# Performance work log

Measured on AMD Instinct MI355X. Metric: run time of the kernel, lower is better.

## Reference

```python
import jax, jax.numpy as jnp
import numpy as np

# Config (matches init_kwargs)
HQ, HKV, HD, WIN = 16, 4, 128, 512  # query heads, kv heads, head_dim, sliding window


def setup_inputs() -> dict:
    key = jax.random.key(0)
    k0, k1, k2, k3, k4 = jax.random.split(key, 5)
    B, S, D = 1, 8192, 2048
    std = 0.02
    hidden_states = jax.random.normal(k0, (B, S, D), jnp.float32)
    Wq = jax.random.normal(k1, (D, HQ * HD), jnp.float32) * std
    Wk = jax.random.normal(k2, (D, HKV * HD), jnp.float32) * std
    Wv = jax.random.normal(k3, (D, HKV * HD), jnp.float32) * std
    Wo = jax.random.normal(k4, (HQ * HD, D), jnp.float32) * std
    return {"hidden_states": hidden_states, "Wq": Wq, "Wk": Wk, "Wv": Wv, "Wo": Wo}


def _sliding_window_attention(q, k, v, win):
    # block i attend to keys of blocks i-1 and i -> scores [B,H,nb,W,2W].
    B, H, S, hd = q.shape
    W = win
    nb = S // W
    qb = q.reshape(B, H, nb, W, hd)
    kpad = jnp.pad(k, ((0, 0), (0, 0), (W, 0), (0, 0)))
    vpad = jnp.pad(v, ((0, 0), (0, 0), (W, 0), (0, 0)))
    kb = jnp.concatenate([kpad[:, :, :S].reshape(B, H, nb, W, hd),
                          k.reshape(B, H, nb, W, hd)], axis=3)  # [B,H,nb,2W,hd]
    vb = jnp.concatenate([vpad[:, :, :S].reshape(B, H, nb, W, hd),
                          v.reshape(B, H, nb, W, hd)], axis=3)
    # Faithful double-scaling of the source: /sqrt(hd) inside the chunk matmul
    # and again before softmax -> effective /hd.
    scores = jnp.einsum('bhnqd,bhnkd->bhnqk', qb, kb) / jnp.asarray(hd, qb.dtype)
    qi = jnp.arange(W)[:, None]
    ki = jnp.arange(2 * W)[None, :]
    # key local index k maps to global offset (k - W) relative to block start;
    # attend iff 0 <= q_glob - k_glob <= W-1  <=>  q+1 <= k <= q+W
    band = (ki >= qi + 1) & (ki <= qi + W)          # [W, 2W]
    blk = jnp.arange(nb)[:, None, None]
    valid = band[None] & ((blk > 0) | (ki[None] >= W))  # block 0 has no prev keys
    neg = jnp.finfo(scores.dtype).min
    scores = jnp.where(valid[None, None], scores, neg)
    probs = jax.nn.softmax(scores, axis=-1)
    out = jnp.einsum('bhnqk,bhnkd->bhnqd', probs, vb)
    return out.reshape(B, H, S, hd)


def reference(hidden_states, Wq, Wk, Wv, Wo):
    B, S, D = hidden_states.shape
    q = (hidden_states @ Wq).reshape(B, S, HQ, HD).transpose(0, 2, 1, 3)
    k = (hidden_states @ Wk).reshape(B, S, HKV, HD).transpose(0, 2, 1, 3)
    v = (hidden_states @ Wv).reshape(B, S, HKV, HD).transpose(0, 2, 1, 3)
    rep = HQ // HKV
    k = jnp.repeat(k, rep, axis=1)
    v = jnp.repeat(v, rep, axis=1)
    attn = _sliding_window_attention(q, k, v, WIN)      # [B,HQ,S,HD]
    attn = attn.transpose(0, 2, 1, 3).reshape(B, S, HQ * HD)
    return attn @ Wo
```

## Files before the change

### kernel.cpp

```cpp
#include <hip/hip_runtime.h>


typedef __bf16 bf16x8 __attribute__((ext_vector_type(8)));
typedef float f32x4 __attribute__((ext_vector_type(4)));
typedef float f32x16 __attribute__((ext_vector_type(16)));
typedef int v8i __attribute__((ext_vector_type(8)));
typedef unsigned int u32x4 __attribute__((ext_vector_type(4)));

__device__ __forceinline__ unsigned short f2bf(float f) {
  unsigned int u = __float_as_uint(f);
  u += 0x7fffu + ((u >> 16) & 1u);
  return (unsigned short)(u >> 16);
}

__device__ __forceinline__ f32x4 mfma16(bf16x8 a, bf16x8 b, f32x4 c) {
  return __builtin_amdgcn_mfma_f32_16x16x32_bf16(a, b, c, 0, 0, 0);
}

__device__ __forceinline__ f32x16 mfma32(bf16x8 a, bf16x8 b, f32x16 c) {
  return __builtin_amdgcn_mfma_f32_32x32x16_bf16(a, b, c, 0, 0, 0);
}

__device__ __forceinline__ unsigned int cvtpk_bf16(float lo, float hi) {
  unsigned int r;
  asm volatile("v_cvt_pk_bf16_f32 %0, %1, %2" : "=v"(r) : "v"(lo), "v"(hi));
  return r;
}

__device__ __forceinline__ void async16(void* lds, const void* g) {
  __builtin_amdgcn_global_load_lds(
      (__attribute__((address_space(1))) unsigned int*)g,
      (__attribute__((address_space(3))) unsigned int*)lds, 16, 0, 0);
}


__global__ __launch_bounds__(256) void convert_h_kernel(
    const float* __restrict__ src, unsigned short* __restrict__ dbf,
    unsigned char* __restrict__ d8, int n) {
  int i = (blockIdx.x * 256 + threadIdx.x) * 4;
  if (i < n) {
    float4 f = *(const float4*)(src + i);
    ushort4 o;
    o.x = f2bf(f.x); o.y = f2bf(f.y); o.z = f2bf(f.z); o.w = f2bf(f.w);
    *(ushort4*)(dbf + i) = o;
    int p = __builtin_amdgcn_cvt_pk_fp8_f32(f.x, f.y, 0, 0);
    p = __builtin_amdgcn_cvt_pk_fp8_f32(f.z, f.w, p, 1);
    *(unsigned int*)(d8 + i) = p;
  }
}

__global__ __launch_bounds__(256) void transpose_convert_kernel(
    const float* __restrict__ src, unsigned short* __restrict__ dst,
    int K, int N) {
  __shared__ unsigned short T[64 * 72];
  int kb = blockIdx.y * 64, nb = blockIdx.x * 64;
  int t = threadIdx.x;
  for (int u = t; u < 1024; u += 256) {
    int r = u >> 4, s = u & 15;
    float4 f = *(const float4*)(src + (size_t)(kb + r) * N + nb + s * 4);
    ushort4 o;
    o.x = f2bf(f.x); o.y = f2bf(f.y); o.z = f2bf(f.z); o.w = f2bf(f.w);
    *(ushort4*)&T[r * 72 + s * 4] = o;
  }
  __syncthreads();
  for (int u = t; u < 1024; u += 256) {
    int orow = u >> 4, s = u & 15;
    ushort4 o;
    o.x = T[(s * 4 + 0) * 72 + orow];
    o.y = T[(s * 4 + 1) * 72 + orow];
    o.z = T[(s * 4 + 2) * 72 + orow];
    o.w = T[(s * 4 + 3) * 72 + orow];
    *(ushort4*)(dst + (size_t)(nb + orow) * K + kb + s * 4) = o;
  }
}

__global__ __launch_bounds__(256) void transpose_convert_fp8_kernel(
    const float* __restrict__ src, unsigned char* __restrict__ dst,
    int K, int N) {
  __shared__ unsigned short T[64 * 72];
  int kb = blockIdx.y * 64, nb = blockIdx.x * 64;
  int t = threadIdx.x;
  for (int u = t; u < 1024; u += 256) {
    int r = u >> 4, s = u & 15;
    float4 f = *(const float4*)(src + (size_t)(kb + r) * N + nb + s * 4);
    ushort4 o;
    o.x = f2bf(f.x); o.y = f2bf(f.y); o.z = f2bf(f.z); o.w = f2bf(f.w);
    *(ushort4*)&T[r * 72 + s * 4] = o;
  }
  __syncthreads();
  for (int u = t; u < 1024; u += 256) {
    int orow = u >> 4, s = u & 15;
    float f0 = __uint_as_float((unsigned int)T[(s * 4 + 0) * 72 + orow] << 16);
    float f1 = __uint_as_float((unsigned int)T[(s * 4 + 1) * 72 + orow] << 16);
    float f2 = __uint_as_float((unsigned int)T[(s * 4 + 2) * 72 + orow] << 16);
    float f3 = __uint_as_float((unsigned int)T[(s * 4 + 3) * 72 + orow] << 16);
    int p = __builtin_amdgcn_cvt_pk_fp8_f32(f0, f1, 0, 0);
    p = __builtin_amdgcn_cvt_pk_fp8_f32(f2, f3, p, 1);
    *(unsigned int*)&dst[(size_t)(nb + orow) * K + kb + s * 4] = p;
  }
}

__global__ __launch_bounds__(256) void vtrans_kernel(
    const unsigned short* __restrict__ QKV, unsigned short* __restrict__ VTg) {
  int flat = blockIdx.x * 256 + threadIdx.x;
  int c = flat & 511;
  int s0 = (flat >> 9) * 8;
  unsigned short tmp[8];
  #pragma unroll
  for (int j = 0; j < 8; ++j)
    tmp[j] = QKV[(size_t)(s0 + j) * 3072 + 2560 + c];
  *(uint4*)&VTg[(size_t)c * 8192 + s0] = *(uint4*)tmp;
}


template <bool F32OUT>
__global__ __launch_bounds__(256) void gemm_bt_kernel(
    const unsigned short* __restrict__ A, const unsigned short* __restrict__ BT,
    void* __restrict__ Cp, int M, int ldc, int K) {
  __shared__ unsigned short As[128 * 32];
  __shared__ unsigned short Bs[128 * 32];
  int mb = blockIdx.y * 128, nb = blockIdx.x * 128;
  int tid = threadIdx.x;
  int lane = tid & 63, wv = tid >> 6;
  int wrow = wv >> 1, wcol = wv & 1;
  int lr = lane >> 2, ls = lane & 3;
  int fr = lane & 15, fg = lane >> 4;
  f32x4 acc[4][4] = {};
  for (int k0 = 0; k0 < K; k0 += 32) {
    __syncthreads();
    #pragma unroll
    for (int r = 0; r < 2; ++r) {
      int s = wv * 2 + r;
      async16(&As[s * 512], &A[(size_t)(mb + s * 16 + lr) * K + k0 + ls * 8]);
      async16(&Bs[s * 512], &BT[(size_t)(nb + s * 16 + lr) * K + k0 + ls * 8]);
    }
    __syncthreads();
    bf16x8 a[4], b[4];
    #pragma unroll
    for (int rt = 0; rt < 4; ++rt)
      a[rt] = *(const bf16x8*)&As[(wrow * 64 + rt * 16 + fr) * 32 + fg * 8];
    #pragma unroll
    for (int ct = 0; ct < 4; ++ct)
      b[ct] = *(const bf16x8*)&Bs[(wcol * 64 + ct * 16 + fr) * 32 + fg * 8];
    #pragma unroll
    for (int rt = 0; rt < 4; ++rt)
      #pragma unroll
      for (int ct = 0; ct < 4; ++ct)
        acc[rt][ct] = mfma16(a[rt], b[ct], acc[rt][ct]);
  }
  #pragma unroll
  for (int rt = 0; rt < 4; ++rt)
    #pragma unroll
    for (int ct = 0; ct < 4; ++ct)
      #pragma unroll
      for (int i = 0; i < 4; ++i) {
        int row = mb + wrow * 64 + rt * 16 + fg * 4 + i;
        int col = nb + wcol * 64 + ct * 16 + fr;
        if constexpr (F32OUT)
          ((float*)Cp)[(size_t)row * ldc + col] = acc[rt][ct][i];
        else
          ((unsigned short*)Cp)[(size_t)row * ldc + col] = f2bf(acc[rt][ct][i]);
      }
}


__global__ __launch_bounds__(512, 2) void gemm8p_oproj_kernel(
    const unsigned short* __restrict__ A, const unsigned short* __restrict__ BT,
    float* __restrict__ C, int ldc, int K) {
  __shared__ unsigned char lds[131072];
  const int mb = blockIdx.y * 256, nb = blockIdx.x * 256;
  const int tid = threadIdx.x;
  const int lane = tid & 63, wv = tid >> 6;
  const int wm = wv >> 2, wn = wv & 3;
  const int fr = lane & 15, fg = lane >> 4;
  const int xr = (fr & 4) ? 32 : 0;
  const int a_base = (wm * 128 + fr) * 128 + ((fg * 16) ^ xr);
  const int b_base = (wn * 64 + fr) * 128 + ((fg * 16) ^ xr);
  const int lsw = (lane * 16) ^ (lane & 32);
  const int lrow = lsw >> 7, lcol = (lsw & 127) >> 1;
  const int NT = K >> 6;

  f32x4 acc[8][4] = {};
  bf16x8 aF[4][2], bF[2][2];

#define FENCE_ asm volatile("" ::: "memory")
#define BAR_ { FENCE_; __builtin_amdgcn_s_barrier(); FENCE_; }
#define LGKM0_ asm volatile("s_waitcnt lgkmcnt(0)" ::: "memory")
#define STAGE_A_(BUFI, T, HALF)                                              \
  { _Pragma("unroll")                                                        \
    for (int l = 0; l < 2; ++l) {                                            \
      int cc = wv * 2 + l;                                                   \
      int rb = (cc >> 3) * 128 + (HALF) * 64 + (cc & 7) * 8;                 \
      async16(lds + (BUFI) * 65536 + rb * 128,                               \
              A + (size_t)(mb + rb + lrow) * K + (T) * 64 + lcol);           \
    } }
#define STAGE_B_(BUFI, T, HALF)                                              \
  { _Pragma("unroll")                                                        \
    for (int l = 0; l < 2; ++l) {                                            \
      int cc = wv * 2 + l;                                                   \
      int rb = (cc >> 2) * 64 + (HALF) * 32 + (cc & 3) * 8;                  \
      async16(lds + (BUFI) * 65536 + 32768 + rb * 128,                       \
              BT + (size_t)(nb + rb + lrow) * K + (T) * 64 + lcol);          \
    } }
#define LOAD_A_(HALF)                                                        \
  { _Pragma("unroll")                                                        \
    for (int q = 0; q < 4; ++q)                                              \
      _Pragma("unroll")                                                      \
      for (int kk = 0; kk < 2; ++kk)                                         \
        aF[q][kk] =                                                          \
            *(const bf16x8*)&Ab_[a_base + ((HALF)*4 + q) * 2048 + kk * 64]; }
#define LOAD_B_(HALF)                                                        \
  { _Pragma("unroll")                                                        \
    for (int c2 = 0; c2 < 2; ++c2)                                           \
      _Pragma("unroll")                                                      \
      for (int kk = 0; kk < 2; ++kk)                                         \
        bF[c2][kk] =                                                         \
            *(const bf16x8*)&Bb_[b_base + ((HALF)*2 + c2) * 2048 + kk * 64]; }
#define MFMA_(RT0, CT0)                                                      \
  { __builtin_amdgcn_s_setprio(1);                                           \
    _Pragma("unroll")                                                        \
    for (int q = 0; q < 4; ++q)                                              \
      _Pragma("unroll")                                                      \
      for (int c2 = 0; c2 < 2; ++c2) {                                       \
        acc[(RT0) + q][(CT0) + c2] =                                         \
            mfma16(aF[q][0], bF[c2][0], acc[(RT0) + q][(CT0) + c2]);         \
        acc[(RT0) + q][(CT0) + c2] =                                         \
            mfma16(aF[q][1], bF[c2][1], acc[(RT0) + q][(CT0) + c2]);         \
      }                                                                      \
    __builtin_amdgcn_s_setprio(0); }

  STAGE_A_(0, 0, 0); STAGE_A_(0, 0, 1); STAGE_B_(0, 0, 0); STAGE_B_(0, 0, 1);
  STAGE_B_(1, 1, 0); STAGE_A_(1, 1, 1);
  asm volatile("s_waitcnt vmcnt(4)" ::: "memory");
  BAR_;

  for (int t = 0; t < NT; ++t) {
    const int cur = t & 1, nxt = cur ^ 1;
    const unsigned char* Ab_ = lds + cur * 65536;
    const unsigned char* Bb_ = Ab_ + 32768;
    LOAD_A_(0); LOAD_B_(0);
    if (t + 1 < NT) STAGE_A_(nxt, t + 1, 0);
    BAR_; LGKM0_;
    MFMA_(0, 0);
    BAR_;
    LOAD_A_(1);
    if (t + 1 < NT) STAGE_B_(nxt, t + 1, 1);
    BAR_; LGKM0_;
    MFMA_(4, 0);
    BAR_;
    LOAD_B_(1);
    if (t + 2 < NT) STAGE_B_(cur, t + 2, 0);
    BAR_; LGKM0_;
    MFMA_(4, 2);
    BAR_;
    LOAD_A_(0);
    if (t + 2 < NT) STAGE_A_(cur, t + 2, 1);
    BAR_; LGKM0_;
    MFMA_(0, 2);
    asm volatile("s_waitcnt vmcnt(4)" ::: "memory");
    BAR_;
  }

  #pragma unroll
  for (int rt = 0; rt < 8; ++rt)
    #pragma unroll
    for (int ct = 0; ct < 4; ++ct)
      #pragma unroll
      for (int i = 0; i < 4; ++i) {
        int row = mb + wm * 128 + rt * 16 + fg * 4 + i;
        int col = nb + wn * 64 + ct * 16 + fr;
        C[(size_t)row * ldc + col] = acc[rt][ct][i];
      }
#undef FENCE_
#undef BAR_
#undef LGKM0_
#undef STAGE_A_
#undef STAGE_B_
#undef LOAD_A_
#undef LOAD_B_
#undef MFMA_
}


__global__ __launch_bounds__(256) void gemm_qk_fp8_kernel(
    const unsigned char* __restrict__ A8, const unsigned char* __restrict__ B8,
    unsigned short* __restrict__ C, int M, int ldc, int K) {
  __shared__ unsigned char As[128 * 144];
  __shared__ unsigned char Bs[128 * 144];
  int mb = blockIdx.y * 128, nb = blockIdx.x * 128;
  int tid = threadIdx.x;
  int lane = tid & 63, wv = tid >> 6;
  int wrow = wv >> 1, wcol = wv & 1;
  int fr = lane & 15, fg = lane >> 4;
  int srow = tid >> 1, shalf = (tid & 1) * 64;
  f32x4 acc[4][4] = {};
  for (int k0 = 0; k0 < K; k0 += 128) {
    __syncthreads();
    #pragma unroll
    for (int j = 0; j < 4; ++j) {
      *(uint4*)&As[srow * 144 + shalf + j * 16] =
          *(const uint4*)&A8[(size_t)(mb + srow) * K + k0 + shalf + j * 16];
      *(uint4*)&Bs[srow * 144 + shalf + j * 16] =
          *(const uint4*)&B8[(size_t)(nb + srow) * K + k0 + shalf + j * 16];
    }
    __syncthreads();
    v8i a[4], b[4];
    #pragma unroll
    for (int rt = 0; rt < 4; ++rt) {
      int off = (wrow * 64 + rt * 16 + fr) * 144 + fg * 32;
      ((uint4*)&a[rt])[0] = *(const uint4*)&As[off];
      ((uint4*)&a[rt])[1] = *(const uint4*)&As[off + 16];
    }
    #pragma unroll
    for (int ct = 0; ct < 4; ++ct) {
      int off = (wcol * 64 + ct * 16 + fr) * 144 + fg * 32;
      ((uint4*)&b[ct])[0] = *(const uint4*)&Bs[off];
      ((uint4*)&b[ct])[1] = *(const uint4*)&Bs[off + 16];
    }
    #pragma unroll
    for (int rt = 0; rt < 4; ++rt)
      #pragma unroll
      for (int ct = 0; ct < 4; ++ct)
        acc[rt][ct] = __builtin_amdgcn_mfma_scale_f32_16x16x128_f8f6f4(
            a[rt], b[ct], acc[rt][ct], 0, 0,
            0, 0x7F7F7F7F,
            0, 0x7F7F7F7F);
  }
  #pragma unroll
  for (int rt = 0; rt < 4; ++rt)
    #pragma unroll
    for (int ct = 0; ct < 4; ++ct)
      #pragma unroll
      for (int i = 0; i < 4; ++i) {
        int row = mb + wrow * 64 + rt * 16 + fg * 4 + i;
        int col = nb + wcol * 64 + ct * 16 + fr;
        C[(size_t)row * ldc + col] = f2bf(acc[rt][ct][i]);
      }
}


#define SCALE_L2E 0.0112710027f

__global__ __launch_bounds__(512, 2) void attn_kernel(
    const unsigned short* __restrict__ QKV,
    const unsigned short* __restrict__ VTg,
    unsigned short* __restrict__ O) {
  __shared__ unsigned short Ks[64 * 136];
  __shared__ unsigned short VTs[128 * 72];
  __shared__ float Ls[8 * 32];
  const int g = blockIdx.y;
  const int qs = blockIdx.x * 64;
  const int tid = threadIdx.x;
  const int lane = tid & 63, w = tid >> 6;
  const int l31 = lane & 31, hl2 = lane >> 5;
  const int hl = w & 3, qh = w >> 2;
  const int h = g * 4 + hl;
  const int kcol = 2048 + g * 128;
  const int qg = qs + qh * 32 + l31;

  bf16x8 qf[8];
  {
    const unsigned short* qrow = &QKV[(size_t)qg * 3072 + h * 128];
    #pragma unroll
    for (int kk = 0; kk < 8; ++kk)
      qf[kk] = *(const bf16x8*)&qrow[kk * 16 + hl2 * 8];
  }

  f32x16 o32[4] = {};
  float l_lane = 0.f;

  const int skey = tid >> 4, sseg = tid & 15;
  const int sd = tid >> 3, sseg2 = tid & 7;

  const int kb0 = qs >= 512 ? qs - 512 : 0;

  {
    uint4 kst[2], vst[2];
    #pragma unroll
    for (int it = 0; it < 2; ++it) {
      kst[it] = *(const uint4*)&QKV[(size_t)(kb0 + skey + it * 32) * 3072 + kcol + sseg * 8];
      vst[it] = *(const uint4*)&VTg[(size_t)(g * 128 + sd + it * 64) * 8192 + kb0 + sseg2 * 8];
    }
    #pragma unroll
    for (int it = 0; it < 2; ++it) {
      *(uint4*)&Ks[(skey + it * 32) * 136 + sseg * 8] = kst[it];
      *(uint4*)&VTs[(sd + it * 64) * 72 + sseg2 * 8] = vst[it];
    }
  }
  __syncthreads();

  for (int kb = kb0; kb <= qs; kb += 64) {
    const bool hasnext = (kb + 64 <= qs);
    uint4 kn[2], vn[2];
    if (hasnext) {
      #pragma unroll
      for (int it = 0; it < 2; ++it) {
        kn[it] = *(const uint4*)&QKV[(size_t)(kb + 64 + skey + it * 32) * 3072 + kcol + sseg * 8];
        vn[it] = *(const uint4*)&VTg[(size_t)(g * 128 + sd + it * 64) * 8192 + kb + 64 + sseg2 * 8];
      }
    }
    f32x16 s32[2] = {};
    __builtin_amdgcn_s_setprio(1);
    #pragma unroll
    for (int kt = 0; kt < 2; ++kt)
      #pragma unroll
      for (int kk = 0; kk < 8; ++kk) {
        bf16x8 kf = *(const bf16x8*)&Ks[(kt * 32 + l31) * 136 + kk * 16 + hl2 * 8];
        s32[kt] = mfma32(kf, qf[kk], s32[kt]);
      }
    __builtin_amdgcn_s_setprio(0);

    const bool edge = (kb > qs - 64) || (kb < qs - 448);
    unsigned int u[2][4][2];
    #pragma unroll
    for (int kt = 0; kt < 2; ++kt) {
      float p[16];
      #pragma unroll
      for (int r = 0; r < 16; ++r) {
        float pv = exp2f(s32[kt][r] * SCALE_L2E);
        if (edge) {
          int kg = kb + kt * 32 + (r & 3) + 8 * (r >> 2) + 4 * hl2;
          if (kg > qg || kg < qg - 511) pv = 0.f;
        }
        l_lane += pv;
        p[r] = pv;
      }
      #pragma unroll
      for (int gr = 0; gr < 4; ++gr) {
        u[kt][gr][0] = cvtpk_bf16(p[4 * gr + 0], p[4 * gr + 1]);
        u[kt][gr][1] = cvtpk_bf16(p[4 * gr + 2], p[4 * gr + 3]);
      }
    }

    bf16x8 af[4];
    #pragma unroll
    for (int kc = 0; kc < 4; ++kc) {
      const int kt = kc >> 1;
      const int gLo = 2 * (kc & 1), gHi = gLo + 1;
      unsigned int xa0 = u[kt][gLo][0], xb0 = u[kt][gHi][0];
      unsigned int xa1 = u[kt][gLo][1], xb1 = u[kt][gHi][1];
      asm volatile("v_permlane32_swap_b32 %0, %1" : "+v"(xa0), "+v"(xb0));
      asm volatile("v_permlane32_swap_b32 %0, %1" : "+v"(xa1), "+v"(xb1));
      u32x4 t;
      t[0] = xa0; t[1] = xa1; t[2] = xb0; t[3] = xb1;
      af[kc] = __builtin_bit_cast(bf16x8, t);
    }

    __builtin_amdgcn_s_setprio(1);
    #pragma unroll
    for (int dc = 0; dc < 4; ++dc)
      #pragma unroll
      for (int kc = 0; kc < 4; ++kc) {
        bf16x8 vf = *(const bf16x8*)&VTs[(dc * 32 + l31) * 72 + kc * 16 + hl2 * 8];
        o32[dc] = mfma32(af[kc], vf, o32[dc]);
      }
    __builtin_amdgcn_s_setprio(0);

    __syncthreads();
    if (hasnext) {
      #pragma unroll
      for (int it = 0; it < 2; ++it) {
        *(uint4*)&Ks[(skey + it * 32) * 136 + sseg * 8] = kn[it];
        *(uint4*)&VTs[(sd + it * 64) * 72 + sseg2 * 8] = vn[it];
      }
      __syncthreads();
    }
  }

  l_lane += __shfl_xor(l_lane, 32);
  float linv = 1.f / l_lane;
  Ls[w * 32 + l31] = linv;
  asm volatile("s_waitcnt lgkmcnt(0)" ::: "memory");
  float lr[16];
  #pragma unroll
  for (int r = 0; r < 16; ++r)
    lr[r] = Ls[w * 32 + (r & 3) + 8 * (r >> 2) + 4 * hl2];
  #pragma unroll
  for (int dc = 0; dc < 4; ++dc)
    #pragma unroll
    for (int r = 0; r < 16; ++r) {
      int row = qs + qh * 32 + (r & 3) + 8 * (r >> 2) + 4 * hl2;
      O[(size_t)row * 2048 + h * 128 + dc * 32 + l31] =
          f2bf(o32[dc][r] * lr[r]);
    }
}


extern "C" void kernel_launch(void* const* d_in, const int* in_sizes, int n_in,
                              void* d_out, int out_size, void* d_ws, size_t ws_size,
                              hipStream_t stream) {
  const float* h  = (const float*)d_in[0];
  const float* Wq = (const float*)d_in[1];
  const float* Wk = (const float*)d_in[2];
  const float* Wv = (const float*)d_in[3];
  const float* Wo = (const float*)d_in[4];
  float* out = (float*)d_out;
  char* ws = (char*)d_ws;
  const int S = 8192, D = 2048;
  const size_t MB = 1024 * 1024;

  unsigned short* QKV = (unsigned short*)(ws);
  unsigned short* hbf = (unsigned short*)(ws + 48 * MB);
  unsigned short* Ab  = hbf;
  unsigned char*  h8  = (unsigned char*)(ws + 80 * MB);
  unsigned short* VTg = (unsigned short*)(ws + 80 * MB);
  unsigned short* WoT = (unsigned short*)(ws + 88 * MB);
  unsigned char*  W8  = (unsigned char*)(ws + 96 * MB);
  unsigned short* WvT = (unsigned short*)(ws + 96 * MB);

  convert_h_kernel<<<16384, 256, 0, stream>>>(h, hbf, h8, S * D);
  transpose_convert_fp8_kernel<<<dim3(32, 32), 256, 0, stream>>>(Wq, W8, D, 2048);
  transpose_convert_fp8_kernel<<<dim3(8, 32), 256, 0, stream>>>(
      Wk, W8 + (size_t)2048 * 2048, D, 512);
  gemm_qk_fp8_kernel<<<dim3(20, 64), 256, 0, stream>>>(h8, W8, QKV, S, 3072, D);

  transpose_convert_kernel<<<dim3(8, 32), 256, 0, stream>>>(Wv, WvT, D, 512);
  gemm_bt_kernel<false><<<dim3(4, 64), 256, 0, stream>>>(hbf, WvT, QKV + 2560, S, 3072, D);

  vtrans_kernel<<<2048, 256, 0, stream>>>(QKV, VTg);
  transpose_convert_kernel<<<dim3(32, 32), 256, 0, stream>>>(Wo, WoT, D, 2048);
  attn_kernel<<<dim3(128, 4), 512, 0, stream>>>(QKV, VTg, Ab);
  gemm8p_oproj_kernel<<<dim3(8, 32), 512, 0, stream>>>(Ab, WoT, out, 2048, 2048);
}
```

Baseline: 446.3 us.

## Double-buffer attention K/V tiles with async global-to-LDS loads and XOR swizzle

The attention kernel's K and V^T shared-memory tiles become double buffered. Each next tile is fetched with async16 global-to-LDS copies while the current tile is being computed, which removes the register staging and the second barrier per iteration. Padded rows are replaced by an XOR-swizzled layout to avoid LDS bank conflicts. This doubles LDS use per block, which could limit occupancy, and it relies on the async copies having completed by the time of the barrier.

```diff
diff --git a/kernel.cpp b/kernel.cpp
--- a/kernel.cpp
+++ b/kernel.cpp
@@ -345,8 +345,8 @@
     const unsigned short* __restrict__ QKV,
     const unsigned short* __restrict__ VTg,
     unsigned short* __restrict__ O) {
-  __shared__ unsigned short Ks[64 * 136];
-  __shared__ unsigned short VTs[128 * 72];
+  __shared__ unsigned short KsL[2 * 64 * 128];
+  __shared__ unsigned short VTsL[2 * 128 * 64];
   __shared__ float Ls[8 * 32];
   const int g = blockIdx.y;
   const int qs = blockIdx.x * 64;
@@ -369,43 +369,44 @@
   f32x16 o32[4] = {};
   float l_lane = 0.f;
 
-  const int skey = tid >> 4, sseg = tid & 15;
-  const int sd = tid >> 3, sseg2 = tid & 7;
+  const int kr_ = w * 4 + (lane >> 4), kc_ = (lane & 15) * 8;
+  const int vr_ = w * 8 + (lane >> 3), vc_ = (lane & 7) * 8;
+
+#define STAGE_TILE_(KB, BI)                                                   \
+  { _Pragma("unroll")                                                         \
+    for (int it = 0; it < 2; ++it) {                                          \
+      int kr = it * 32 + kr_;                                                 \
+      async16(&KsL[(BI) * 8192 + it * 4096 + w * 512],                        \
+              &QKV[(size_t)((KB) + kr) * 3072 + kcol +                        \
+                   (kc_ ^ ((kr & 7) << 3))]);                                 \
+      int vr = it * 64 + vr_;                                                 \
+      async16(&VTsL[(BI) * 8192 + it * 4096 + w * 512],                       \
+              &VTg[(size_t)(g * 128 + vr) * 8192 + (KB) +                     \
+                   (vc_ ^ ((vr & 7) << 3))]);                                 \
+    } }
 
   const int kb0 = qs >= 512 ? qs - 512 : 0;
 
-  {
-    uint4 kst[2], vst[2];
-    #pragma unroll
-    for (int it = 0; it < 2; ++it) {
-      kst[it] = *(const uint4*)&QKV[(size_t)(kb0 + skey + it * 32) * 3072 + kcol + sseg * 8];
-      vst[it] = *(const uint4*)&VTg[(size_t)(g * 128 + sd + it * 64) * 8192 + kb0 + sseg2 * 8];
-    }
-    #pragma unroll
-    for (int it = 0; it < 2; ++it) {
-      *(uint4*)&Ks[(skey + it * 32) * 136 + sseg * 8] = kst[it];
-      *(uint4*)&VTs[(sd + it * 64) * 72 + sseg2 * 8] = vst[it];
-    }
-  }
+  STAGE_TILE_(kb0, 0);
   __syncthreads();
 
+  int cur = 0;
   for (int kb = kb0; kb <= qs; kb += 64) {
     const bool hasnext = (kb + 64 <= qs);
-    uint4 kn[2], vn[2];
-    if (hasnext) {
-      #pragma unroll
-      for (int it = 0; it < 2; ++it) {
-        kn[it] = *(const uint4*)&QKV[(size_t)(kb + 64 + skey + it * 32) * 3072 + kcol + sseg * 8];
-        vn[it] = *(const uint4*)&VTg[(size_t)(g * 128 + sd + it * 64) * 8192 + kb + 64 + sseg2 * 8];
-      }
-    }
+    if (hasnext) STAGE_TILE_(kb + 64, cur ^ 1);
+
+    const unsigned short* Kc = &KsL[cur * 8192];
+    const unsigned short* Vc = &VTsL[cur * 8192];
+
     f32x16 s32[2] = {};
     __builtin_amdgcn_s_setprio(1);
     #pragma unroll
     for (int kt = 0; kt < 2; ++kt)
       #pragma unroll
       for (int kk = 0; kk < 8; ++kk) {
-        bf16x8 kf = *(const bf16x8*)&Ks[(kt * 32 + l31) * 136 + kk * 16 + hl2 * 8];
+        int row = kt * 32 + l31;
+        bf16x8 kf = *(const bf16x8*)
+            &Kc[row * 128 + ((kk * 16 + hl2 * 8) ^ ((row & 7) << 3))];
         s32[kt] = mfma32(kf, qf[kk], s32[kt]);
       }
     __builtin_amdgcn_s_setprio(0);
@@ -451,20 +452,15 @@
     for (int dc = 0; dc < 4; ++dc)
       #pragma unroll
       for (int kc = 0; kc < 4; ++kc) {
-        bf16x8 vf = *(const bf16x8*)&VTs[(dc * 32 + l31) * 72 + kc * 16 + hl2 * 8];
+        int row = dc * 32 + l31;
+        bf16x8 vf = *(const bf16x8*)
+            &Vc[row * 64 + ((kc * 16 + hl2 * 8) ^ ((row & 7) << 3))];
         o32[dc] = mfma32(af[kc], vf, o32[dc]);
       }
     __builtin_amdgcn_s_setprio(0);
 
     __syncthreads();
-    if (hasnext) {
-      #pragma unroll
-      for (int it = 0; it < 2; ++it) {
-        *(uint4*)&Ks[(skey + it * 32) * 136 + sseg * 8] = kn[it];
-        *(uint4*)&VTs[(sd + it * 64) * 72 + sseg2 * 8] = vn[it];
-      }
-      __syncthreads();
-    }
+    cur ^= 1;
   }
 
   l_lane += __shfl_xor(l_lane, 32);
@@ -483,6 +479,7 @@
       O[(size_t)row * 2048 + h * 128 + dc * 32 + l31] =
           f2bf(o32[dc][r] * lr[r]);
     }
+#undef STAGE_TILE_
 }
 
 
```

Result: faster. 422.2 us (-5.4%).
